# Optimization experiments

Measured on AMD Instinct MI355X. Metric: run time of the kernel, lower is better.

## Reference

```python
import jax, jax.numpy as jnp
import numpy as np

B, NH, T, D = 2, 16, 2048, 64

def setup_inputs() -> dict:
    key = jax.random.key(0)
    kq, kk, kv = jax.random.split(key, 3)
    Q = jax.random.normal(kq, (B, NH, T, D), dtype=jnp.float32)
    K = jax.random.normal(kk, (B, NH, T, D), dtype=jnp.float32)
    V = jax.random.normal(kv, (B, NH, T, D), dtype=jnp.float32)
    return {"Q": Q, "K": K, "V": V}

def reference(Q, K, V):
    # scores: [B, nh, T, T]
    Dh = Q.shape[-1]
    scale = 1.0 / jnp.sqrt(jnp.asarray(Dh, Q.dtype))
    scores = jnp.einsum('bhtd,bhsd->bhts', Q, K) * scale
    Tq = Q.shape[2]
    causal = jnp.tril(jnp.ones((Tq, Tq), dtype=bool))
    scores = jnp.where(causal, scores, jnp.asarray(-jnp.inf, scores.dtype))
    attn = jax.nn.softmax(scores, axis=-1)
    return jnp.einsum('bhts,bhsd->bhtd', attn, V)
```

## Files before the change

### kernel.cpp

```cpp
#include <hip/hip_runtime.h>
#include <hip/hip_bf16.h>


typedef __bf16 bf16;
typedef __bf16 bf16x8 __attribute__((ext_vector_type(8)));
typedef float floatx4 __attribute__((ext_vector_type(4)));

#define T_SEQ 2048
#define DH 64
#define TQ 64
#define TK 64
#define NQT (T_SEQ / TQ)
#define BHN 32
#define CEXP 0.18033688011112042f

__device__ __forceinline__ void gload16(const bf16* g, bf16* l) {
    __builtin_amdgcn_global_load_lds(
        (const __attribute__((address_space(1))) void*)g,
        (__attribute__((address_space(3))) void*)l, 16, 0, 0);
}

__global__ __launch_bounds__(256) void cvt_k(const float* __restrict__ in,
                                             bf16* __restrict__ out) {
    const int i = ((int)blockIdx.x * 256 + (int)threadIdx.x) * 8;
    float4 a = *(const float4*)(in + i);
    float4 b = *(const float4*)(in + i + 4);
    bf16x8 o;
    o[0] = (bf16)a.x; o[1] = (bf16)a.y; o[2] = (bf16)a.z; o[3] = (bf16)a.w;
    o[4] = (bf16)b.x; o[5] = (bf16)b.y; o[6] = (bf16)b.z; o[7] = (bf16)b.w;
    *(bf16x8*)(out + i) = o;
}

__global__ __launch_bounds__(256) void transpose_v(const float* __restrict__ V,
                                                   bf16* __restrict__ Vt) {
    __shared__ bf16 tile[64][72];
    const int bh = (int)blockIdx.x & (BHN - 1);
    const int t0 = ((int)blockIdx.x >> 5) * 64;
    const int tid = (int)threadIdx.x;
    {
        const int r = tid >> 2;
        const int c = (tid & 3) * 16;
        const float* s = V + ((size_t)(bh * T_SEQ) + t0 + r) * DH + c;
        float4 f0 = *(const float4*)(s + 0);
        float4 f1 = *(const float4*)(s + 4);
        float4 f2 = *(const float4*)(s + 8);
        float4 f3 = *(const float4*)(s + 12);
        bf16x8 p0, p1;
        p0[0] = (bf16)f0.x; p0[1] = (bf16)f0.y; p0[2] = (bf16)f0.z; p0[3] = (bf16)f0.w;
        p0[4] = (bf16)f1.x; p0[5] = (bf16)f1.y; p0[6] = (bf16)f1.z; p0[7] = (bf16)f1.w;
        p1[0] = (bf16)f2.x; p1[1] = (bf16)f2.y; p1[2] = (bf16)f2.z; p1[3] = (bf16)f2.w;
        p1[4] = (bf16)f3.x; p1[5] = (bf16)f3.y; p1[6] = (bf16)f3.z; p1[7] = (bf16)f3.w;
        *(bf16x8*)&tile[r][c + 0] = p0;
        *(bf16x8*)&tile[r][c + 8] = p1;
    }
    __syncthreads();
    {
        const int d  = tid & 63;
        const int k0 = (tid >> 6) * 16;
        bf16x8 o0, o1;
        #pragma unroll
        for (int j = 0; j < 8; ++j) { o0[j] = tile[k0 + j][d]; o1[j] = tile[k0 + 8 + j][d]; }
        bf16* o = Vt + ((size_t)bh * DH + d) * T_SEQ + t0 + k0;
        *(bf16x8*)(o + 0) = o0;
        *(bf16x8*)(o + 8) = o1;
    }
}

__global__ __launch_bounds__(256, 4)
void fa_fwd(const float* __restrict__ Qg, const bf16* __restrict__ Kb,
            const bf16* __restrict__ Vt, float* __restrict__ Og)
{
    __shared__ __align__(16) bf16 Ksh[2][TK * DH];
    __shared__ __align__(16) bf16 Vsh[2][DH * TK];
    __shared__ __align__(16) bf16 Psh[4][16 * TK];

    const int gid  = (int)blockIdx.x;
    const int bh   = gid & (BHN - 1);
    const int qt   = (NQT - 1) - (gid >> 5);
    const int q0   = qt * TQ;

    const int tid  = (int)threadIdx.x;
    const int wave = tid >> 6;
    const int lane = tid & 63;
    const int quad = lane >> 4;
    const int l16  = lane & 15;
    const int rl   = lane >> 3;
    const int ch   = lane & 7;
    const int gch  = ch ^ rl;

    const float* Qb  = Qg + ((size_t)bh * T_SEQ + q0) * DH;
    const bf16*  Kbh = Kb + (size_t)bh * T_SEQ * DH;
    const bf16*  Vbh = Vt + (size_t)bh * DH * T_SEQ;
    float*       Ob  = Og + ((size_t)bh * T_SEQ + q0) * DH;

    bf16x8 qa[2];
    {
        const float* s0 = Qb + (size_t)(wave * 16 + l16) * DH + quad * 8;
        #pragma unroll
        for (int kk = 0; kk < 2; ++kk) {
            const float* s = s0 + kk * 32;
            float4 f0 = *(const float4*)(s);
            float4 f1 = *(const float4*)(s + 4);
            bf16x8 t;
            t[0] = (bf16)f0.x; t[1] = (bf16)f0.y; t[2] = (bf16)f0.z; t[3] = (bf16)f0.w;
            t[4] = (bf16)f1.x; t[5] = (bf16)f1.y; t[6] = (bf16)f1.z; t[7] = (bf16)f1.w;
            qa[kk] = t;
        }
    }

    floatx4 oacc[4];
    #pragma unroll
    for (int dt = 0; dt < 4; ++dt) oacc[dt] = (floatx4){0.f, 0.f, 0.f, 0.f};
    float l_part[4] = {0.f, 0.f, 0.f, 0.f};

    auto stage = [&](int kt, int buf) {
        const bf16* kg = Kbh + (size_t)kt * TK * DH;
        const bf16* vg = Vbh + kt * TK;
        #pragma unroll
        for (int g = 0; g < 2; ++g) {
            const int row = wave * 16 + g * 8;
            gload16(kg + (size_t)(row + rl) * DH + gch * 8, &Ksh[buf][row * DH]);
            gload16(vg + (size_t)(row + rl) * T_SEQ + gch * 8, &Vsh[buf][row * TK]);
        }
    };

    stage(0, 0);
    __syncthreads();

    for (int kt = 0; kt <= qt; ++kt) {
        const int buf = kt & 1;
        if (kt < qt) stage(kt + 1, buf ^ 1);

        floatx4 sacc[4];
        #pragma unroll
        for (int nt = 0; nt < 4; ++nt) sacc[nt] = (floatx4){0.f, 0.f, 0.f, 0.f};
        #pragma unroll
        for (int nt = 0; nt < 4; ++nt) {
            const int R = nt * 16 + l16;
            #pragma unroll
            for (int kk = 0; kk < 2; ++kk) {
                bf16x8 b = *(const bf16x8*)&Ksh[buf][R * DH + (((kk * 4 + quad) ^ (l16 & 7)) * 8)];
                sacc[nt] = __builtin_amdgcn_mfma_f32_16x16x32_bf16(qa[kk], b, sacc[nt], 0, 0, 0);
            }
        }

        if (kt == qt) {
            #pragma unroll
            for (int nt = 0; nt < 4; ++nt) {
                const int ng = nt * 16 + l16;
                #pragma unroll
                for (int r = 0; r < 4; ++r) {
                    const int mg = wave * 16 + quad * 4 + r;
                    if (ng > mg) sacc[nt][r] = -INFINITY;
                }
            }
        }

        bf16* Pw = Psh[wave];
        #pragma unroll
        for (int nt = 0; nt < 4; ++nt) {
            const int key = nt * 16 + l16;
            #pragma unroll
            for (int r = 0; r < 4; ++r) {
                const float p = __builtin_amdgcn_exp2f(CEXP * sacc[nt][r]);
                l_part[r] += p;
                const int qrow = quad * 4 + r;
                Pw[qrow * TK + (((key >> 3) ^ (qrow & 7)) * 8 + (key & 7))] = (bf16)p;
            }
        }

        bf16x8 pa[2];
        #pragma unroll
        for (int kk = 0; kk < 2; ++kk)
            pa[kk] = *(const bf16x8*)&Pw[l16 * TK + (((kk * 4 + quad) ^ (l16 & 7)) * 8)];

        #pragma unroll
        for (int dt = 0; dt < 4; ++dt) {
            const int R = dt * 16 + l16;
            #pragma unroll
            for (int kk = 0; kk < 2; ++kk) {
                bf16x8 vb = *(const bf16x8*)&Vsh[buf][R * TK + (((kk * 4 + quad) ^ (l16 & 7)) * 8)];
                oacc[dt] = __builtin_amdgcn_mfma_f32_16x16x32_bf16(pa[kk], vb, oacc[dt], 0, 0, 0);
            }
        }

        __syncthreads();
    }

    float inv_l[4];
    #pragma unroll
    for (int r = 0; r < 4; ++r) {
        float v = l_part[r];
        #pragma unroll
        for (int msk = 1; msk <= 8; msk <<= 1) v += __shfl_xor(v, msk);
        inv_l[r] = 1.0f / v;
    }

    #pragma unroll
    for (int dt = 0; dt < 4; ++dt) {
        #pragma unroll
        for (int r = 0; r < 4; ++r) {
            const int row = wave * 16 + quad * 4 + r;
            Ob[(size_t)row * DH + dt * 16 + l16] = oacc[dt][r] * inv_l[r];
        }
    }
}

extern "C" void kernel_launch(void* const* d_in, const int* in_sizes, int n_in,
                              void* d_out, int out_size, void* d_ws, size_t ws_size,
                              hipStream_t stream) {
    const float* Q = (const float*)d_in[0];
    const float* K = (const float*)d_in[1];
    const float* V = (const float*)d_in[2];
    float* O = (float*)d_out;
    (void)in_sizes; (void)n_in; (void)out_size; (void)ws_size;

    const size_t nelem = (size_t)BHN * T_SEQ * DH;
    bf16* Kbf = (bf16*)d_ws;
    bf16* Vtb = Kbf + nelem;

    cvt_k<<<dim3((unsigned)(nelem / (256 * 8))), dim3(256), 0, stream>>>(K, Kbf);
    transpose_v<<<dim3(BHN * (T_SEQ / 64)), dim3(256), 0, stream>>>(V, Vtb);
    fa_fwd<<<dim3(BHN * NQT), dim3(256), 0, stream>>>(Q, Kbf, Vtb, O);
}
```

Before: 134.1 us.

## Use 128-row query tiles with transposed S=K·Q MFMA and fuse prep kernels

Each attention block now covers 128 query rows, with each wave handling 32 rows, so every staged K/V tile is reused across twice as many queries. The score MFMA is computed as K·Q^T so the P values can be written to LDS as 4-wide vectors and the output stored as float4. The K conversion and V transpose kernels are merged into one launch, and query tiles are ordered so heavy and light causal tiles are paired across the grid. This raises register and LDS use per block (launch bounds drop to 2 blocks per CU) and halves the number of attention blocks to 512, which may reduce latency hiding.

```diff
diff --git a/kernel.cpp b/kernel.cpp
--- a/kernel.cpp
+++ b/kernel.cpp
@@ -3,12 +3,13 @@
 
 
 typedef __bf16 bf16;
+typedef __bf16 bf16x4 __attribute__((ext_vector_type(4)));
 typedef __bf16 bf16x8 __attribute__((ext_vector_type(8)));
 typedef float floatx4 __attribute__((ext_vector_type(4)));
 
 #define T_SEQ 2048
 #define DH 64
-#define TQ 64
+#define TQ 128
 #define TK 64
 #define NQT (T_SEQ / TQ)
 #define BHN 32
@@ -20,64 +21,76 @@
         (__attribute__((address_space(3))) void*)l, 16, 0, 0);
 }
 
-__global__ __launch_bounds__(256) void cvt_k(const float* __restrict__ in,
-                                             bf16* __restrict__ out) {
-    const int i = ((int)blockIdx.x * 256 + (int)threadIdx.x) * 8;
-    float4 a = *(const float4*)(in + i);
-    float4 b = *(const float4*)(in + i + 4);
-    bf16x8 o;
-    o[0] = (bf16)a.x; o[1] = (bf16)a.y; o[2] = (bf16)a.z; o[3] = (bf16)a.w;
-    o[4] = (bf16)b.x; o[5] = (bf16)b.y; o[6] = (bf16)b.z; o[7] = (bf16)b.w;
-    *(bf16x8*)(out + i) = o;
-}
-
-__global__ __launch_bounds__(256) void transpose_v(const float* __restrict__ V,
-                                                   bf16* __restrict__ Vt) {
+__global__ __launch_bounds__(256) void prep(const float* __restrict__ K,
+                                            const float* __restrict__ V,
+                                            bf16* __restrict__ Kb,
+                                            bf16* __restrict__ Vt) {
+    const int bid = (int)blockIdx.x;
+    const int tid = (int)threadIdx.x;
+    if (bid < 1024) {
+        const size_t i = ((size_t)bid * 256 + tid) * 16;
+        float4 a = *(const float4*)(K + i + 0);
+        float4 b = *(const float4*)(K + i + 4);
+        float4 c = *(const float4*)(K + i + 8);
+        float4 d = *(const float4*)(K + i + 12);
+        bf16x8 o0, o1;
+        o0[0]=(bf16)a.x; o0[1]=(bf16)a.y; o0[2]=(bf16)a.z; o0[3]=(bf16)a.w;
+        o0[4]=(bf16)b.x; o0[5]=(bf16)b.y; o0[6]=(bf16)b.z; o0[7]=(bf16)b.w;
+        o1[0]=(bf16)c.x; o1[1]=(bf16)c.y; o1[2]=(bf16)c.z; o1[3]=(bf16)c.w;
+        o1[4]=(bf16)d.x; o1[5]=(bf16)d.y; o1[6]=(bf16)d.z; o1[7]=(bf16)d.w;
+        *(bf16x8*)(Kb + i + 0) = o0;
+        *(bf16x8*)(Kb + i + 8) = o1;
+        return;
+    }
     __shared__ bf16 tile[64][72];
-    const int bh = (int)blockIdx.x & (BHN - 1);
-    const int t0 = ((int)blockIdx.x >> 5) * 64;
-    const int tid = (int)threadIdx.x;
+    const int vb = bid - 1024;
+    const int bh = vb & (BHN - 1);
+    const int t0 = (vb >> 5) * 64;
     {
         const int r = tid >> 2;
         const int c = (tid & 3) * 16;
-        const float* s = V + ((size_t)(bh * T_SEQ) + t0 + r) * DH + c;
+        const float* s = V + ((size_t)bh * T_SEQ + t0 + r) * DH + c;
         float4 f0 = *(const float4*)(s + 0);
         float4 f1 = *(const float4*)(s + 4);
         float4 f2 = *(const float4*)(s + 8);
         float4 f3 = *(const float4*)(s + 12);
         bf16x8 p0, p1;
-        p0[0] = (bf16)f0.x; p0[1] = (bf16)f0.y; p0[2] = (bf16)f0.z; p0[3] = (bf16)f0.w;
-        p0[4] = (bf16)f1.x; p0[5] = (bf16)f1.y; p0[6] = (bf16)f1.z; p0[7] = (bf16)f1.w;
-        p1[0] = (bf16)f2.x; p1[1] = (bf16)f2.y; p1[2] = (bf16)f2.z; p1[3] = (bf16)f2.w;
-        p1[4] = (bf16)f3.x; p1[5] = (bf16)f3.y; p1[6] = (bf16)f3.z; p1[7] = (bf16)f3.w;
+        p0[0]=(bf16)f0.x; p0[1]=(bf16)f0.y; p0[2]=(bf16)f0.z; p0[3]=(bf16)f0.w;
+        p0[4]=(bf16)f1.x; p0[5]=(bf16)f1.y; p0[6]=(bf16)f1.z; p0[7]=(bf16)f1.w;
+        p1[0]=(bf16)f2.x; p1[1]=(bf16)f2.y; p1[2]=(bf16)f2.z; p1[3]=(bf16)f2.w;
+        p1[4]=(bf16)f3.x; p1[5]=(bf16)f3.y; p1[6]=(bf16)f3.z; p1[7]=(bf16)f3.w;
         *(bf16x8*)&tile[r][c + 0] = p0;
         *(bf16x8*)&tile[r][c + 8] = p1;
     }
     __syncthreads();
     {
-        const int d  = tid & 63;
-        const int k0 = (tid >> 6) * 16;
+        const int d   = tid >> 2;
+        const int tch = (tid & 3) * 16;
         bf16x8 o0, o1;
         #pragma unroll
-        for (int j = 0; j < 8; ++j) { o0[j] = tile[k0 + j][d]; o1[j] = tile[k0 + 8 + j][d]; }
-        bf16* o = Vt + ((size_t)bh * DH + d) * T_SEQ + t0 + k0;
+        for (int j = 0; j < 8; ++j) { o0[j] = tile[tch + j][d]; o1[j] = tile[tch + 8 + j][d]; }
+        bf16* o = Vt + ((size_t)bh * DH + d) * T_SEQ + t0 + tch;
         *(bf16x8*)(o + 0) = o0;
         *(bf16x8*)(o + 8) = o1;
     }
 }
 
-__global__ __launch_bounds__(256, 4)
+__global__ __launch_bounds__(256, 2)
 void fa_fwd(const float* __restrict__ Qg, const bf16* __restrict__ Kb,
             const bf16* __restrict__ Vt, float* __restrict__ Og)
 {
     __shared__ __align__(16) bf16 Ksh[2][TK * DH];
     __shared__ __align__(16) bf16 Vsh[2][DH * TK];
-    __shared__ __align__(16) bf16 Psh[4][16 * TK];
+    __shared__ __align__(16) bf16 Psh[4][32 * TK];
 
     const int gid  = (int)blockIdx.x;
-    const int bh   = gid & (BHN - 1);
-    const int qt   = (NQT - 1) - (gid >> 5);
-    const int q0   = qt * TQ;
+    const int pair = gid & 255;
+    const int half = gid >> 8;
+    const int bh   = pair & (BHN - 1);
+    const int ip   = pair >> 5;
+    const int iq   = half ? ip : (NQT - 1 - ip);
+    const int q0   = iq * TQ;
+    const int nkt  = 2 * iq + 2;
 
     const int tid  = (int)threadIdx.x;
     const int wave = tid >> 6;
@@ -85,33 +98,35 @@
     const int quad = lane >> 4;
     const int l16  = lane & 15;
     const int rl   = lane >> 3;
-    const int ch   = lane & 7;
-    const int gch  = ch ^ rl;
-
-    const float* Qb  = Qg + ((size_t)bh * T_SEQ + q0) * DH;
-    const bf16*  Kbh = Kb + (size_t)bh * T_SEQ * DH;
-    const bf16*  Vbh = Vt + (size_t)bh * DH * T_SEQ;
-    float*       Ob  = Og + ((size_t)bh * T_SEQ + q0) * DH;
-
-    bf16x8 qa[2];
-    {
-        const float* s0 = Qb + (size_t)(wave * 16 + l16) * DH + quad * 8;
+    const int gch  = (lane & 7) ^ rl;
+
+    const bf16* Kbh = Kb + (size_t)bh * T_SEQ * DH;
+    const bf16* Vbh = Vt + (size_t)bh * DH * T_SEQ;
+
+    const int qw = q0 + wave * 32;
+
+    bf16x8 qb[2][2];
+    #pragma unroll
+    for (int nt = 0; nt < 2; ++nt) {
+        const int qrow = qw + nt * 16 + l16;
         #pragma unroll
         for (int kk = 0; kk < 2; ++kk) {
-            const float* s = s0 + kk * 32;
+            const float* s = Qg + ((size_t)bh * T_SEQ + qrow) * DH + kk * 32 + quad * 8;
             float4 f0 = *(const float4*)(s);
             float4 f1 = *(const float4*)(s + 4);
             bf16x8 t;
-            t[0] = (bf16)f0.x; t[1] = (bf16)f0.y; t[2] = (bf16)f0.z; t[3] = (bf16)f0.w;
-            t[4] = (bf16)f1.x; t[5] = (bf16)f1.y; t[6] = (bf16)f1.z; t[7] = (bf16)f1.w;
-            qa[kk] = t;
-        }
-    }
-
-    floatx4 oacc[4];
-    #pragma unroll
-    for (int dt = 0; dt < 4; ++dt) oacc[dt] = (floatx4){0.f, 0.f, 0.f, 0.f};
-    float l_part[4] = {0.f, 0.f, 0.f, 0.f};
+            t[0]=(bf16)f0.x; t[1]=(bf16)f0.y; t[2]=(bf16)f0.z; t[3]=(bf16)f0.w;
+            t[4]=(bf16)f1.x; t[5]=(bf16)f1.y; t[6]=(bf16)f1.z; t[7]=(bf16)f1.w;
+            qb[nt][kk] = t;
+        }
+    }
+
+    floatx4 oacc[4][2];
+    #pragma unroll
+    for (int mt = 0; mt < 4; ++mt)
+        #pragma unroll
+        for (int nt = 0; nt < 2; ++nt) oacc[mt][nt] = (floatx4){0.f,0.f,0.f,0.f};
+    float lpart[2] = {0.f, 0.f};
 
     auto stage = [&](int kt, int buf) {
         const bf16* kg = Kbh + (size_t)kt * TK * DH;
@@ -127,81 +142,105 @@
     stage(0, 0);
     __syncthreads();
 
-    for (int kt = 0; kt <= qt; ++kt) {
+    for (int kt = 0; kt < nkt; ++kt) {
         const int buf = kt & 1;
-        if (kt < qt) stage(kt + 1, buf ^ 1);
-
-        floatx4 sacc[4];
-        #pragma unroll
-        for (int nt = 0; nt < 4; ++nt) sacc[nt] = (floatx4){0.f, 0.f, 0.f, 0.f};
-        #pragma unroll
-        for (int nt = 0; nt < 4; ++nt) {
-            const int R = nt * 16 + l16;
-            #pragma unroll
-            for (int kk = 0; kk < 2; ++kk) {
-                bf16x8 b = *(const bf16x8*)&Ksh[buf][R * DH + (((kk * 4 + quad) ^ (l16 & 7)) * 8)];
-                sacc[nt] = __builtin_amdgcn_mfma_f32_16x16x32_bf16(qa[kk], b, sacc[nt], 0, 0, 0);
-            }
-        }
-
-        if (kt == qt) {
-            #pragma unroll
-            for (int nt = 0; nt < 4; ++nt) {
-                const int ng = nt * 16 + l16;
+        const int k0  = kt * TK;
+        if (kt + 1 < nkt) stage(kt + 1, buf ^ 1);
+
+        floatx4 sacc[4][2];
+        #pragma unroll
+        for (int mt = 0; mt < 4; ++mt)
+            #pragma unroll
+            for (int nt = 0; nt < 2; ++nt) sacc[mt][nt] = (floatx4){0.f,0.f,0.f,0.f};
+        #pragma unroll
+        for (int kk = 0; kk < 2; ++kk) {
+            #pragma unroll
+            for (int mt = 0; mt < 4; ++mt) {
+                const int R = mt * 16 + l16;
+                bf16x8 kf = *(const bf16x8*)&Ksh[buf][R * DH + (((kk * 4 + quad) ^ (l16 & 7)) * 8)];
+                #pragma unroll
+                for (int nt = 0; nt < 2; ++nt)
+                    sacc[mt][nt] = __builtin_amdgcn_mfma_f32_16x16x32_bf16(kf, qb[nt][kk], sacc[mt][nt], 0, 0, 0);
+            }
+        }
+
+        if (k0 + TK - 1 > qw) {
+            #pragma unroll
+            for (int mt = 0; mt < 4; ++mt) {
+                #pragma unroll
+                for (int nt = 0; nt < 2; ++nt) {
+                    const int qg = qw + nt * 16 + l16;
+                    #pragma unroll
+                    for (int r = 0; r < 4; ++r) {
+                        const int keyg = k0 + mt * 16 + quad * 4 + r;
+                        if (keyg > qg) sacc[mt][nt][r] = -INFINITY;
+                    }
+                }
+            }
+        }
+
+        bf16* Pw = Psh[wave];
+        #pragma unroll
+        for (int mt = 0; mt < 4; ++mt) {
+            #pragma unroll
+            for (int nt = 0; nt < 2; ++nt) {
+                bf16x4 w;
                 #pragma unroll
                 for (int r = 0; r < 4; ++r) {
-                    const int mg = wave * 16 + quad * 4 + r;
-                    if (ng > mg) sacc[nt][r] = -INFINITY;
+                    const float p = __builtin_amdgcn_exp2f(CEXP * sacc[mt][nt][r]);
+                    lpart[nt] += p;
+                    w[r] = (bf16)p;
                 }
-            }
-        }
-
-        bf16* Pw = Psh[wave];
-        #pragma unroll
-        for (int nt = 0; nt < 4; ++nt) {
-            const int key = nt * 16 + l16;
-            #pragma unroll
-            for (int r = 0; r < 4; ++r) {
-                const float p = __builtin_amdgcn_exp2f(CEXP * sacc[nt][r]);
-                l_part[r] += p;
-                const int qrow = quad * 4 + r;
-                Pw[qrow * TK + (((key >> 3) ^ (qrow & 7)) * 8 + (key & 7))] = (bf16)p;
-            }
-        }
-
-        bf16x8 pa[2];
-        #pragma unroll
-        for (int kk = 0; kk < 2; ++kk)
-            pa[kk] = *(const bf16x8*)&Pw[l16 * TK + (((kk * 4 + quad) ^ (l16 & 7)) * 8)];
-
-        #pragma unroll
-        for (int dt = 0; dt < 4; ++dt) {
-            const int R = dt * 16 + l16;
-            #pragma unroll
-            for (int kk = 0; kk < 2; ++kk) {
-                bf16x8 vb = *(const bf16x8*)&Vsh[buf][R * TK + (((kk * 4 + quad) ^ (l16 & 7)) * 8)];
-                oacc[dt] = __builtin_amdgcn_mfma_f32_16x16x32_bf16(pa[kk], vb, oacc[dt], 0, 0, 0);
+                const int row = nt * 16 + l16;
+                const int c   = (mt * 2 + (quad >> 1)) ^ (row & 7);
+                *(bf16x4*)&Pw[row * TK + c * 8 + (quad & 1) * 4] = w;
+            }
+        }
+
+        bf16x8 pf[2][2];
+        #pragma unroll
+        for (int nt = 0; nt < 2; ++nt) {
+            const int row = nt * 16 + l16;
+            #pragma unroll
+            for (int kk = 0; kk < 2; ++kk)
+                pf[nt][kk] = *(const bf16x8*)&Pw[row * TK + (((kk * 4 + quad) ^ (row & 7)) * 8)];
+        }
+
+        #pragma unroll
+        for (int kk = 0; kk < 2; ++kk) {
+            #pragma unroll
+            for (int mt = 0; mt < 4; ++mt) {
+                const int R = mt * 16 + l16;
+                bf16x8 vf = *(const bf16x8*)&Vsh[buf][R * TK + (((kk * 4 + quad) ^ (l16 & 7)) * 8)];
+                #pragma unroll
+                for (int nt = 0; nt < 2; ++nt)
+                    oacc[mt][nt] = __builtin_amdgcn_mfma_f32_16x16x32_bf16(vf, pf[nt][kk], oacc[mt][nt], 0, 0, 0);
             }
         }
 
         __syncthreads();
     }
 
-    float inv_l[4];
-    #pragma unroll
-    for (int r = 0; r < 4; ++r) {
-        float v = l_part[r];
-        #pragma unroll
-        for (int msk = 1; msk <= 8; msk <<= 1) v += __shfl_xor(v, msk);
-        inv_l[r] = 1.0f / v;
-    }
-
-    #pragma unroll
-    for (int dt = 0; dt < 4; ++dt) {
-        #pragma unroll
-        for (int r = 0; r < 4; ++r) {
-            const int row = wave * 16 + quad * 4 + r;
-            Ob[(size_t)row * DH + dt * 16 + l16] = oacc[dt][r] * inv_l[r];
+    float invl[2];
+    #pragma unroll
+    for (int nt = 0; nt < 2; ++nt) {
+        float v = lpart[nt];
+        v += __shfl_xor(v, 16);
+        v += __shfl_xor(v, 32);
+        invl[nt] = 1.0f / v;
+    }
+
+    #pragma unroll
+    for (int nt = 0; nt < 2; ++nt) {
+        const size_t qrow = (size_t)bh * T_SEQ + qw + nt * 16 + l16;
+        #pragma unroll
+        for (int mt = 0; mt < 4; ++mt) {
+            float4 o;
+            o.x = oacc[mt][nt][0] * invl[nt];
+            o.y = oacc[mt][nt][1] * invl[nt];
+            o.z = oacc[mt][nt][2] * invl[nt];
+            o.w = oacc[mt][nt][3] * invl[nt];
+            *(float4*)&Og[qrow * DH + mt * 16 + quad * 4] = o;
         }
     }
 }
@@ -219,7 +258,6 @@
     bf16* Kbf = (bf16*)d_ws;
     bf16* Vtb = Kbf + nelem;
 
-    cvt_k<<<dim3((unsigned)(nelem / (256 * 8))), dim3(256), 0, stream>>>(K, Kbf);
-    transpose_v<<<dim3(BHN * (T_SEQ / 64)), dim3(256), 0, stream>>>(V, Vtb);
-    fa_fwd<<<dim3(BHN * NQT), dim3(256), 0, stream>>>(Q, Kbf, Vtb, O);
-}
+    prep<<<dim3(2048), dim3(256), 0, stream>>>(K, V, Kbf, Vtb);
+    fa_fwd<<<dim3(512), dim3(256), 0, stream>>>(Q, Kbf, Vtb, O);
+}
```

Measured after the change: 137.8 us. 2.7% more time.
